# Optimization experiments

Measured on AMD Instinct MI355X. Metric: run time of the kernel, lower is better.

The kernel has to match this reference:

```python
import jax, jax.numpy as jnp
import numpy as np


def setup_inputs() -> dict:
    key = jax.random.key(0)
    ks = jax.random.split(key, 7)
    B, C, H, W = 32, 512, 64, 64
    C8 = C // 8
    scale = 1.0 / np.sqrt(C)  # ~kaiming-ish for 1x1 conv
    return {
        "x": jax.random.normal(ks[0], (B, C, H, W), dtype=jnp.float32),
        "wq": jax.random.normal(ks[1], (C8, C), dtype=jnp.float32) * scale,
        "bq": jax.random.normal(ks[2], (C8,), dtype=jnp.float32) * 0.01,
        "wk": jax.random.normal(ks[3], (C8, C), dtype=jnp.float32) * scale,
        "bk": jax.random.normal(ks[4], (C8,), dtype=jnp.float32) * 0.01,
        "wv": jax.random.normal(ks[5], (C8, C), dtype=jnp.float32) * scale,
        "bv": jax.random.normal(ks[6], (C8,), dtype=jnp.float32) * 0.01,
    }


def reference(x, wq, bq, wk, bk, wv, bv):
    B, C, H, W = x.shape
    N = H * W
    xf = x.reshape(B, C, N)  # [B, C, N]
    # 1x1 convs == per-pixel linear projections C -> C//8
    q = jnp.einsum("bcn,oc->bon", xf, wq) + bq[None, :, None]  # [B, C8, N]
    k = jnp.einsum("bcn,oc->bon", xf, wk) + bk[None, :, None]  # [B, C8, N]
    v = jnp.einsum("bcn,oc->bon", xf, wv) + bv[None, :, None]  # [B, C8, N]
    # attention over channel pairs: [B, C8, C8], softmax over dim=-2 (rows)
    logits = jnp.einsum("bon,bpn->bop", q, k)
    attn = jax.nn.softmax(logits, axis=-2)
    out = jnp.einsum("bop,bpn->bon", attn, v)  # [B, C8, N]
    return out.mean(axis=-1)  # [B, C8]
```

## Files before the change

### kernel.cpp

```cpp
#include <hip/hip_runtime.h>


typedef __attribute__((ext_vector_type(8))) short short8;
typedef __attribute__((ext_vector_type(4))) float floatx4;

#define MFMA16(a, b, c) __builtin_amdgcn_mfma_f32_16x16x32_bf16((a), (b), (c), 0, 0, 0)

__device__ __forceinline__ unsigned short f2bf(float f) {
  unsigned int u = __float_as_uint(f);
  u = u + 0x7fffu + ((u >> 16) & 1u);
  return (unsigned short)(u >> 16);
}
__device__ __forceinline__ float bf2f(unsigned short h) {
  return __uint_as_float(((unsigned int)h) << 16);
}

constexpr int CB = 32;
constexpr int CC = 512;
constexpr int CO = 64;
constexpr int NN = 4096;
constexpr int QROW = 72;

constexpr int ZERO_CNT = CB * CO * CO + CB * CO;
constexpr int WMAT  = 16 * 64 * 32;

__global__ __launch_bounds__(256) void zero_kernel(float* __restrict__ p, int n) {
  const int i = blockIdx.x * 256 + threadIdx.x;
  if (i < n) p[i] = 0.0f;
}

__global__ __launch_bounds__(256) void prep_w_kernel(
    const float* __restrict__ wq, const float* __restrict__ wk,
    const float* __restrict__ wv, unsigned short* __restrict__ ws5)
{
  const int gid = blockIdx.x * 256 + threadIdx.x;
#pragma unroll
  for (int e = 0; e < 2; ++e) {
    const int idx = e * 16384 + gid;
    const int o = idx >> 9, c = idx & 511;
    const int dst = ((c >> 5) * 64 + o) * 32 + (c & 31);
    const float q = wq[idx], k = wk[idx], v = wv[idx];
    const unsigned short qh = f2bf(q), kh = f2bf(k);
    ws5[dst]             = qh;
    ws5[dst + WMAT]      = f2bf(q - bf2f(qh));
    ws5[dst + 2 * WMAT]  = kh;
    ws5[dst + 3 * WMAT]  = f2bf(k - bf2f(kh));
    ws5[dst + 4 * WMAT]  = f2bf(v);
  }
}

__global__ __launch_bounds__(256, 2) void proj_kernel(
    const float* __restrict__ x, const unsigned short* __restrict__ ws5,
    const float* __restrict__ bq, const float* __restrict__ bk,
    float* __restrict__ logits, float* __restrict__ vsum)
{
  __shared__ __align__(16) unsigned short smem[4 * 64 * QROW];
  __shared__ float vps[4][64];

  const int t    = threadIdx.x;
  const int lane = t & 63;
  const int wave = t >> 6;
  const int quad = lane >> 4;
  const int l15  = lane & 15;
  const int b    = blockIdx.x >> 5;
  const int tile = blockIdx.x & 31;

  floatx4 accq[4][2], acck[4][2], accv[4][2];
#pragma unroll
  for (int mf = 0; mf < 4; ++mf)
#pragma unroll
    for (int nf = 0; nf < 2; ++nf) {
      accq[mf][nf] = (floatx4)0.0f;
      acck[mf][nf] = (floatx4)0.0f;
      accv[mf][nf] = (floatx4)0.0f;
    }

  const float* xp = x + (size_t)b * CC * NN + (size_t)(quad * 8) * NN
                      + tile * 128 + wave * 32 + l15;

  auto load_x = [&](float xv[2][8], const float* p) {
#pragma unroll
    for (int j = 0; j < 8; ++j) {
      xv[0][j] = p[(size_t)j * NN];
      xv[1][j] = p[(size_t)j * NN + 16];
    }
  };

  auto compute = [&](const float xv[2][8], int ch) {
    short8 xh[2], xl[2];
#pragma unroll
    for (int nf = 0; nf < 2; ++nf)
#pragma unroll
      for (int j = 0; j < 8; ++j) {
        const unsigned short h = f2bf(xv[nf][j]);
        xh[nf][j] = (short)h;
        xl[nf][j] = (short)f2bf(xv[nf][j] - bf2f(h));
      }
    const unsigned short* wch = ws5 + ch * 2048 + l15 * 32 + quad * 8;
#pragma unroll
    for (int mf = 0; mf < 4; ++mf) {
      const unsigned short* wo = wch + mf * 512;
      const short8 aqh = *reinterpret_cast<const short8*>(wo);
      const short8 aql = *reinterpret_cast<const short8*>(wo + WMAT);
      const short8 akh = *reinterpret_cast<const short8*>(wo + 2 * WMAT);
      const short8 akl = *reinterpret_cast<const short8*>(wo + 3 * WMAT);
      const short8 avh = *reinterpret_cast<const short8*>(wo + 4 * WMAT);
#pragma unroll
      for (int nf = 0; nf < 2; ++nf) {
        accq[mf][nf] = MFMA16(aqh, xh[nf], accq[mf][nf]);
        accq[mf][nf] = MFMA16(aql, xh[nf], accq[mf][nf]);
        accq[mf][nf] = MFMA16(aqh, xl[nf], accq[mf][nf]);
        acck[mf][nf] = MFMA16(akh, xh[nf], acck[mf][nf]);
        acck[mf][nf] = MFMA16(akl, xh[nf], acck[mf][nf]);
        acck[mf][nf] = MFMA16(akh, xl[nf], acck[mf][nf]);
        accv[mf][nf] = MFMA16(avh, xh[nf], accv[mf][nf]);
      }
    }
  };

  float xv0[2][8], xv1[2][8];
  load_x(xv0, xp); xp += (size_t)32 * NN;
  for (int ch = 0; ch < 14; ch += 2) {
    load_x(xv1, xp); xp += (size_t)32 * NN;
    compute(xv0, ch);
    load_x(xv0, xp); xp += (size_t)32 * NN;
    compute(xv1, ch + 1);
  }
  load_x(xv1, xp);
  compute(xv0, 14);
  compute(xv1, 15);

#pragma unroll
  for (int mf = 0; mf < 4; ++mf)
#pragma unroll
    for (int r = 0; r < 4; ++r) {
      const int o = mf * 16 + quad * 4 + r;
      const float bqv = bq[o], bkv = bk[o];
#pragma unroll
      for (int nf = 0; nf < 2; ++nf) {
        accq[mf][nf][r] += bqv;
        acck[mf][nf][r] += bkv;
      }
    }

  constexpr int QHI = 0, QLO = 4608, KHI = 9216, KLO = 13824;
  floatx4 accS[4];
#pragma unroll
  for (int mf = 0; mf < 4; ++mf) accS[mf] = (floatx4)0.0f;

  for (int hh = 0; hh < 2; ++hh) {
    __syncthreads();
    if ((wave >> 1) == hh) {
      const int nbase = (wave & 1) * 32;
#pragma unroll
      for (int mf = 0; mf < 4; ++mf)
#pragma unroll
        for (int nf = 0; nf < 2; ++nf)
#pragma unroll
          for (int r = 0; r < 4; ++r) {
            const int o  = mf * 16 + quad * 4 + r;
            const int nc = nbase + nf * 16 + l15;
            const float qv = accq[mf][nf][r];
            const float kv = acck[mf][nf][r];
            const unsigned short qh = f2bf(qv);
            const unsigned short kh = f2bf(kv);
            smem[QHI + o * QROW + nc] = qh;
            smem[QLO + o * QROW + nc] = f2bf(qv - bf2f(qh));
            smem[KHI + o * QROW + nc] = kh;
            smem[KLO + o * QROW + nc] = f2bf(kv - bf2f(kh));
          }
    }
    __syncthreads();
#pragma unroll
    for (int ks = 0; ks < 2; ++ks) {
      const short8 bh = *reinterpret_cast<const short8*>(
          &smem[KHI + (wave * 16 + l15) * QROW + ks * 32 + quad * 8]);
      const short8 bl = *reinterpret_cast<const short8*>(
          &smem[KLO + (wave * 16 + l15) * QROW + ks * 32 + quad * 8]);
#pragma unroll
      for (int mf = 0; mf < 4; ++mf) {
        const short8 ah = *reinterpret_cast<const short8*>(
            &smem[QHI + (mf * 16 + l15) * QROW + ks * 32 + quad * 8]);
        const short8 al = *reinterpret_cast<const short8*>(
            &smem[QLO + (mf * 16 + l15) * QROW + ks * 32 + quad * 8]);
        accS[mf] = MFMA16(ah, bh, accS[mf]);
        accS[mf] = MFMA16(al, bh, accS[mf]);
        accS[mf] = MFMA16(ah, bl, accS[mf]);
      }
    }
  }

#pragma unroll
  for (int mf = 0; mf < 4; ++mf)
#pragma unroll
    for (int r = 0; r < 4; ++r) {
      const int o = mf * 16 + quad * 4 + r;
      const int p = wave * 16 + l15;
      atomicAdd(&logits[((size_t)b * CO + o) * CO + p], accS[mf][r]);
    }

#pragma unroll
  for (int mf = 0; mf < 4; ++mf)
#pragma unroll
    for (int r = 0; r < 4; ++r) {
      float sv = accv[mf][0][r] + accv[mf][1][r];
      sv += __shfl_xor(sv, 1); sv += __shfl_xor(sv, 2);
      sv += __shfl_xor(sv, 4); sv += __shfl_xor(sv, 8);
      if (l15 == 0) vps[wave][mf * 16 + quad * 4 + r] = sv;
    }
  __syncthreads();
  if (t < CO) {
    const float s = vps[0][t] + vps[1][t] + vps[2][t] + vps[3][t];
    atomicAdd(&vsum[b * CO + t], s);
  }
}

__global__ __launch_bounds__(256) void finalize_kernel(
    const float* __restrict__ bv, const float* __restrict__ logits,
    const float* __restrict__ vsum, float* __restrict__ out)
{
  __shared__ float ls[CO * 65];
  __shared__ float w2_s[CO], cmax_s[CO];
  const int t = threadIdx.x;
  const int b = blockIdx.x;

#pragma unroll
  for (int i = 0; i < 16; ++i) {
    const int idx = t + i * 256;
    ls[(idx >> 6) * 65 + (idx & 63)] = logits[(size_t)b * CO * CO + idx];
  }
  __syncthreads();

  if (t < CO) {
    float m = -1e30f;
    for (int o = 0; o < CO; ++o) m = fmaxf(m, ls[o * 65 + t]);
    float sum = 0.f;
    for (int o = 0; o < CO; ++o) sum += __expf(ls[o * 65 + t] - m);
    cmax_s[t] = m;
    const float vbar = vsum[b * CO + t] * (1.0f / 4096.0f) + bv[t];
    w2_s[t] = vbar / sum;
  }
  __syncthreads();

  if (t < CO) {
    float acc = 0.f;
    for (int p = 0; p < CO; ++p)
      acc += __expf(ls[t * 65 + p] - cmax_s[p]) * w2_s[p];
    out[b * CO + t] = acc;
  }
}

extern "C" void kernel_launch(void* const* d_in, const int* in_sizes, int n_in,
                              void* d_out, int out_size, void* d_ws, size_t ws_size,
                              hipStream_t stream) {
  const float* x  = (const float*)d_in[0];
  const float* wq = (const float*)d_in[1];
  const float* bq = (const float*)d_in[2];
  const float* wk = (const float*)d_in[3];
  const float* bk = (const float*)d_in[4];
  const float* wv = (const float*)d_in[5];
  const float* bv = (const float*)d_in[6];
  float* out = (float*)d_out;

  float* logits = (float*)d_ws;
  float* vsum   = logits + CB * CO * CO;
  unsigned short* ws5 = (unsigned short*)(vsum + CB * CO);

  zero_kernel<<<(ZERO_CNT + 255) / 256, 256, 0, stream>>>(logits, ZERO_CNT);
  prep_w_kernel<<<64, 256, 0, stream>>>(wq, wk, wv, ws5);
  proj_kernel<<<CB * 32, 256, 0, stream>>>(x, ws5, bq, bk, logits, vsum);
  finalize_kernel<<<CB, 256, 0, stream>>>(bv, logits, vsum, out);
}
```

Measured before the change: 414.2 us.

## Fuse setup kernels and fold finalize into last block via atomic counter

```diff
diff --git a/kernel.cpp b/kernel.cpp
--- a/kernel.cpp
+++ b/kernel.cpp
@@ -21,41 +21,46 @@
 constexpr int NN = 4096;
 constexpr int QROW = 72;
 
-constexpr int ZERO_CNT = CB * CO * CO + CB * CO;
-constexpr int WMAT  = 16 * 64 * 32;
-
-__global__ __launch_bounds__(256) void zero_kernel(float* __restrict__ p, int n) {
-  const int i = blockIdx.x * 256 + threadIdx.x;
-  if (i < n) p[i] = 0.0f;
-}
-
-__global__ __launch_bounds__(256) void prep_w_kernel(
+constexpr int ZERO_TOT = CB * CO * CO + CB * CO + CB;
+constexpr int WMAT = 16 * 64 * 32;
+
+__global__ __launch_bounds__(256) void setup_kernel(
     const float* __restrict__ wq, const float* __restrict__ wk,
-    const float* __restrict__ wv, unsigned short* __restrict__ ws5)
+    const float* __restrict__ wv, float* __restrict__ zbase,
+    unsigned short* __restrict__ ws5)
 {
-  const int gid = blockIdx.x * 256 + threadIdx.x;
-#pragma unroll
-  for (int e = 0; e < 2; ++e) {
-    const int idx = e * 16384 + gid;
-    const int o = idx >> 9, c = idx & 511;
-    const int dst = ((c >> 5) * 64 + o) * 32 + (c & 31);
-    const float q = wq[idx], k = wk[idx], v = wv[idx];
-    const unsigned short qh = f2bf(q), kh = f2bf(k);
-    ws5[dst]             = qh;
-    ws5[dst + WMAT]      = f2bf(q - bf2f(qh));
-    ws5[dst + 2 * WMAT]  = kh;
-    ws5[dst + 3 * WMAT]  = f2bf(k - bf2f(kh));
-    ws5[dst + 4 * WMAT]  = f2bf(v);
+  const int blk = blockIdx.x;
+  const int t = threadIdx.x;
+  if (blk < 64) {
+    const int gid = blk * 256 + t;
+#pragma unroll
+    for (int e = 0; e < 2; ++e) {
+      const int idx = e * 16384 + gid;
+      const int o = idx >> 9, c = idx & 511;
+      const int dst = ((c >> 5) * 64 + o) * 32 + (c & 31);
+      const float q = wq[idx], k = wk[idx], v = wv[idx];
+      const unsigned short qh = f2bf(q), kh = f2bf(k);
+      ws5[dst]            = qh;
+      ws5[dst + WMAT]     = f2bf(q - bf2f(qh));
+      ws5[dst + 2 * WMAT] = kh;
+      ws5[dst + 3 * WMAT] = f2bf(k - bf2f(kh));
+      ws5[dst + 4 * WMAT] = f2bf(v);
+    }
+  } else {
+    for (int i = (blk - 64) * 256 + t; i < ZERO_TOT; i += 64 * 256)
+      zbase[i] = 0.0f;
   }
 }
 
 __global__ __launch_bounds__(256, 2) void proj_kernel(
     const float* __restrict__ x, const unsigned short* __restrict__ ws5,
     const float* __restrict__ bq, const float* __restrict__ bk,
-    float* __restrict__ logits, float* __restrict__ vsum)
+    const float* __restrict__ bv, float* __restrict__ logits,
+    float* __restrict__ vsum, int* __restrict__ cnt, float* __restrict__ out)
 {
   __shared__ __align__(16) unsigned short smem[4 * 64 * QROW];
   __shared__ float vps[4][64];
+  __shared__ int is_last;
 
   const int t    = threadIdx.x;
   const int lane = t & 63;
@@ -78,16 +83,15 @@
   const float* xp = x + (size_t)b * CC * NN + (size_t)(quad * 8) * NN
                       + tile * 128 + wave * 32 + l15;
 
-  auto load_x = [&](float xv[2][8], const float* p) {
+  float xv[2][8];
+  auto load_x = [&](const float* p) {
 #pragma unroll
     for (int j = 0; j < 8; ++j) {
       xv[0][j] = p[(size_t)j * NN];
       xv[1][j] = p[(size_t)j * NN + 16];
     }
   };
-
-  auto compute = [&](const float xv[2][8], int ch) {
-    short8 xh[2], xl[2];
+  auto cvt = [&](short8 xh[2], short8 xl[2]) {
 #pragma unroll
     for (int nf = 0; nf < 2; ++nf)
 #pragma unroll
@@ -96,6 +100,8 @@
         xh[nf][j] = (short)h;
         xl[nf][j] = (short)f2bf(xv[nf][j] - bf2f(h));
       }
+  };
+  auto compute = [&](const short8 xh[2], const short8 xl[2], int ch) {
     const unsigned short* wch = ws5 + ch * 2048 + l15 * 32 + quad * 8;
 #pragma unroll
     for (int mf = 0; mf < 4; ++mf) {
@@ -118,17 +124,21 @@
     }
   };
 
-  float xv0[2][8], xv1[2][8];
-  load_x(xv0, xp); xp += (size_t)32 * NN;
+  short8 xh0[2], xl0[2], xh1[2], xl1[2];
+  load_x(xp); xp += (size_t)32 * NN;
+  cvt(xh0, xl0);
   for (int ch = 0; ch < 14; ch += 2) {
-    load_x(xv1, xp); xp += (size_t)32 * NN;
-    compute(xv0, ch);
-    load_x(xv0, xp); xp += (size_t)32 * NN;
-    compute(xv1, ch + 1);
-  }
-  load_x(xv1, xp);
-  compute(xv0, 14);
-  compute(xv1, 15);
+    load_x(xp); xp += (size_t)32 * NN;
+    compute(xh0, xl0, ch);
+    cvt(xh1, xl1);
+    load_x(xp); xp += (size_t)32 * NN;
+    compute(xh1, xl1, ch + 1);
+    cvt(xh0, xl0);
+  }
+  load_x(xp);
+  compute(xh0, xl0, 14);
+  cvt(xh1, xl1);
+  compute(xh1, xl1, 15);
 
 #pragma unroll
   for (int mf = 0; mf < 4; ++mf)
@@ -213,32 +223,37 @@
     const float s = vps[0][t] + vps[1][t] + vps[2][t] + vps[3][t];
     atomicAdd(&vsum[b * CO + t], s);
   }
-}
-
-__global__ __launch_bounds__(256) void finalize_kernel(
-    const float* __restrict__ bv, const float* __restrict__ logits,
-    const float* __restrict__ vsum, float* __restrict__ out)
-{
-  __shared__ float ls[CO * 65];
-  __shared__ float w2_s[CO], cmax_s[CO];
-  const int t = threadIdx.x;
-  const int b = blockIdx.x;
-
+
+  __syncthreads();
+  if (t == 0) {
+    __threadfence();
+    const int old = __hip_atomic_fetch_add(&cnt[b], 1, __ATOMIC_ACQ_REL,
+                                           __HIP_MEMORY_SCOPE_AGENT);
+    is_last = (old == CB - 1) ? 1 : 0;
+  }
+  __syncthreads();
+  if (!is_last) return;
+
+  float* ls = reinterpret_cast<float*>(smem);
 #pragma unroll
   for (int i = 0; i < 16; ++i) {
     const int idx = t + i * 256;
-    ls[(idx >> 6) * 65 + (idx & 63)] = logits[(size_t)b * CO * CO + idx];
-  }
-  __syncthreads();
-
+    const float v = __hip_atomic_load(&logits[(size_t)b * CO * CO + idx],
+                                      __ATOMIC_RELAXED, __HIP_MEMORY_SCOPE_AGENT);
+    ls[(idx >> 6) * 65 + (idx & 63)] = v;
+  }
+  __syncthreads();
+
+  __shared__ float w2_s[CO], cmax_s[CO];
   if (t < CO) {
     float m = -1e30f;
     for (int o = 0; o < CO; ++o) m = fmaxf(m, ls[o * 65 + t]);
     float sum = 0.f;
     for (int o = 0; o < CO; ++o) sum += __expf(ls[o * 65 + t] - m);
     cmax_s[t] = m;
-    const float vbar = vsum[b * CO + t] * (1.0f / 4096.0f) + bv[t];
-    w2_s[t] = vbar / sum;
+    const float vs = __hip_atomic_load(&vsum[b * CO + t], __ATOMIC_RELAXED,
+                                       __HIP_MEMORY_SCOPE_AGENT);
+    w2_s[t] = (vs * (1.0f / 4096.0f) + bv[t]) / sum;
   }
   __syncthreads();
 
@@ -264,10 +279,10 @@
 
   float* logits = (float*)d_ws;
   float* vsum   = logits + CB * CO * CO;
-  unsigned short* ws5 = (unsigned short*)(vsum + CB * CO);
-
-  zero_kernel<<<(ZERO_CNT + 255) / 256, 256, 0, stream>>>(logits, ZERO_CNT);
-  prep_w_kernel<<<64, 256, 0, stream>>>(wq, wk, wv, ws5);
-  proj_kernel<<<CB * 32, 256, 0, stream>>>(x, ws5, bq, bk, logits, vsum);
-  finalize_kernel<<<CB, 256, 0, stream>>>(bv, logits, vsum, out);
-}
+  int*   cnt    = (int*)(vsum + CB * CO);
+  unsigned short* ws5 = (unsigned short*)(cnt + CB);
+
+  setup_kernel<<<128, 256, 0, stream>>>(wq, wk, wv, logits, ws5);
+  proj_kernel<<<CB * 32, 256, 0, stream>>>(x, ws5, bq, bk, bv, logits, vsum,
+                                           cnt, out);
+}
```

After: 526.6 us. 1.27x slower.
